# Optimization experiments

Hardware: AMD Instinct MI355X
Metric: run time of the kernel (lower is better)

Reference implementation:

```python
import jax, jax.numpy as jnp
import numpy as np

N = 50000      # nodes
E = 800000     # edges (avg degree 16)
B = 8          # graphs in batch
H = 128        # hidden (message_passer out_channels)
FF = 64        # fourier_feat_dim -> fourier features have dim 2*FF
REPEATS = 4    # repeats_training
OUT = 4        # output_dim
IN_X = 5
IN_MASK = 3

def _fourier(x, M):
    # https://arxiv.org/pdf/2106.02795.pdf : [cos(xM), sin(xM)] / sqrt(2F)
    p = x @ M
    return jnp.concatenate([jnp.cos(p), jnp.sin(p)], axis=-1) / jnp.sqrt(2.0 * M.shape[1])

def _seg_mean(v, idx, n):
    s = jax.ops.segment_sum(v, idx, num_segments=n)
    c = jax.ops.segment_sum(jnp.ones((v.shape[0],), v.dtype), idx, num_segments=n)
    return s / jnp.maximum(c, 1.0)[:, None]

def setup_inputs() -> dict:
    key = jax.random.key(0)
    ks = jax.random.split(key, 16)
    x = jax.random.normal(ks[0], (N, IN_X), jnp.float32)
    x_mask = jax.random.bernoulli(ks[1], 0.1, (N, IN_MASK)).astype(jnp.float32)
    edge_index = jax.random.randint(ks[2], (2, E), 0, N)
    edge_attr = jax.random.normal(ks[3], (E, 3), jnp.float32)
    pos = jax.random.uniform(ks[4], (N, 2), jnp.float32)
    batch = jnp.sort(jax.random.randint(ks[5], (N,), 0, B))
    sampling_points = jax.random.uniform(ks[6], (2,), jnp.float32)
    fourier_mat = jax.random.normal(ks[7], (2, FF), jnp.float32)  # learnable, init N(0,1)
    W_enc = jax.random.normal(ks[8], (IN_X + IN_MASK, H), jnp.float32) * 0.1
    b_enc = jnp.zeros((H,), jnp.float32)
    W_msg = jax.random.normal(ks[9], (2 * H + 3, H), jnp.float32) * 0.05
    b_msg = jnp.zeros((H,), jnp.float32)
    W_upd = jax.random.normal(ks[10], (4 * H, H), jnp.float32) * 0.05
    b_upd = jnp.zeros((H,), jnp.float32)
    W_dec = jax.random.normal(ks[11], (H, OUT), jnp.float32) * 0.1
    b_dec = jnp.zeros((OUT,), jnp.float32)
    return dict(x=x, x_mask=x_mask, edge_index=edge_index, edge_attr=edge_attr,
                pos=pos, batch=batch, sampling_points=sampling_points,
                fourier_mat=fourier_mat, W_enc=W_enc, b_enc=b_enc,
                W_msg=W_msg, b_msg=b_msg, W_upd=W_upd, b_upd=b_upd,
                W_dec=W_dec, b_dec=b_dec)

def reference(x, x_mask, edge_index, edge_attr, pos, batch, sampling_points,
              fourier_mat, W_enc, b_enc, W_msg, b_msg, W_upd, b_upd, W_dec, b_dec):
    bc = x_mask[:, -1]                                   # 0/1 BC flag
    x_full = jnp.concatenate([x, x_mask], axis=1)        # x = concat([x, x_mask])
    keys_ff = _fourier(pos, fourier_mat)                 # input fourier features [N, 2F]
    h = jax.nn.relu(x_full @ W_enc + b_enc)              # encoder -> [N, H]

    # x_BC: scatter-mean over BC nodes per graph (computed once)
    bc_sum = jax.ops.segment_sum(h * bc[:, None], batch, num_segments=B)
    bc_cnt = jax.ops.segment_sum(bc, batch, num_segments=B)
    x_BC = bc_sum / jnp.maximum(bc_cnt, 1.0)[:, None]    # [B, H]

    x_graph = _seg_mean(h, batch, B)                     # global_mean_pool [B, H]
    src, dst = edge_index[0], edge_index[1]
    deg = jnp.maximum(jax.ops.segment_sum(jnp.ones((E,), h.dtype), dst, num_segments=N), 1.0)

    for _ in range(REPEATS):  # repeated message passing
        m = jax.nn.relu(jnp.concatenate([h[src], h[dst], edge_attr], axis=1) @ W_msg + b_msg)
        agg = jax.ops.segment_sum(m, dst, num_segments=N) / deg[:, None]  # scatter-mean
        upd_in = jnp.concatenate([h, agg, x_graph[batch], x_BC[batch]], axis=1)
        h = h + jax.nn.relu(upd_in @ W_upd + b_upd)
        x_graph = _seg_mean(h, batch, B)                 # re-pool each repeat

    decoded = h @ W_dec + b_dec                          # [N, OUT]

    # kernelized fourier-feature interpolation at the sampling point
    q = _fourier(sampling_points, fourier_mat)           # [2F]
    nq = q / jnp.linalg.norm(q)
    nk = keys_ff / jnp.linalg.norm(keys_ff, axis=1, keepdims=True)
    vals_sum = h.sum(axis=0)                             # [H]
    kwv = nk.T @ h                                       # [2F, H]
    ks_sum = nk.sum(axis=0)                              # [2F]
    enc = (vals_sum + nq @ kwv) / (N + nq @ ks_sum)      # [H]
    U_sampled = enc @ W_dec + b_dec                      # [OUT]
    # pack (U_sampled, decoded) into one array: row 0 = sampled point, rows 1: = nodes
    return jnp.concatenate([U_sampled[None, :], decoded], axis=0)
```

## Files before the change

kernel.cpp:

```cpp
#include <hip/hip_runtime.h>
#include <math.h>

#define Nn 50000
#define Ee 800000
#define Bb 8
#define ROUNDS 4
#define KWVB 512
#define SCB 196
#define AP 40
#define HP 132
#define KS 40

typedef __attribute__((ext_vector_type(8))) short bf16x8;
typedef __attribute__((ext_vector_type(4))) float f32x4;

__device__ inline short f2bf(float f) {
  union { float f; unsigned u; } v; v.f = f;
  unsigned r = v.u + 0x7fff + ((v.u >> 16) & 1);
  return (short)(r >> 16);
}
__device__ inline float bf2f(short s) {
  union { float f; unsigned u; } v; v.u = ((unsigned)(unsigned short)s) << 16;
  return v.f;
}

__global__ __launch_bounds__(256) void encode_seg(
    const float* __restrict__ x, const float* __restrict__ xm,
    const int* __restrict__ batch, const float* __restrict__ W,
    const float* __restrict__ b, float* __restrict__ h,
    float* __restrict__ gsum, float* __restrict__ gcnt,
    float* __restrict__ bcsum, float* __restrict__ bccnt) {
  __shared__ float xs5[128 * 5];
  __shared__ float xm3[128 * 3];
  __shared__ float ls[Bb * 128];
  __shared__ float lb[Bb * 128];
  __shared__ float lc[Bb], lbc[Bb];
  const int t = threadIdx.x;
  const int nBase = blockIdx.x * 128;
  const int j = t & 127, half = t >> 7;
  const int base5 = nBase * 5, base3 = nBase * 3;
  for (int q = t; q < 640; q += 256) xs5[q] = (base5 + q < Nn * 5) ? x[base5 + q] : 0.f;
  for (int q = t; q < 384; q += 256) xm3[q] = (base3 + q < Nn * 3) ? xm[base3 + q] : 0.f;
  for (int q = t; q < Bb * 128; q += 256) { ls[q] = 0.f; lb[q] = 0.f; }
  if (t < Bb) { lc[t] = 0.f; lbc[t] = 0.f; }
  float Wcol[8];
#pragma unroll
  for (int k = 0; k < 8; k++) Wcol[k] = W[k * 128 + j];
  const float bj = b[j];
  __syncthreads();
  int curb = -1;
  float runh = 0.f, runb = 0.f, runc = 0.f, runbc = 0.f;
  for (int kk = 0; kk < 64; kk++) {
    int i = nBase + kk * 2 + half;
    if (i >= Nn) break;
    int li = i - nBase;
    float acc = bj;
#pragma unroll
    for (int k = 0; k < 5; k++) acc = fmaf(xs5[li * 5 + k], Wcol[k], acc);
#pragma unroll
    for (int k = 0; k < 3; k++) acc = fmaf(xm3[li * 3 + k], Wcol[5 + k], acc);
    float v = fmaxf(acc, 0.f);
    h[(size_t)i * 128 + j] = v;
    float bc = xm3[li * 3 + 2];
    int g = batch[i];
    if (g != curb) {
      if (curb >= 0) {
        atomicAdd(&ls[curb * 128 + j], runh);
        atomicAdd(&lb[curb * 128 + j], runb);
        if (j == 0) { atomicAdd(&lc[curb], runc); atomicAdd(&lbc[curb], runbc); }
      }
      curb = g; runh = runb = runc = runbc = 0.f;
    }
    runh += v; runb += v * bc;
    if (j == 0) { runc += 1.f; runbc += bc; }
  }
  if (curb >= 0) {
    atomicAdd(&ls[curb * 128 + j], runh);
    atomicAdd(&lb[curb * 128 + j], runb);
    if (j == 0) { atomicAdd(&lc[curb], runc); atomicAdd(&lbc[curb], runbc); }
  }
  __syncthreads();
  for (int q = t; q < Bb * 128; q += 256) {
    float a = ls[q], c = lb[q];
    if (a != 0.f) atomicAdd(&gsum[q], a);
    if (c != 0.f) atomicAdd(&bcsum[q], c);
  }
  if (t < Bb) { atomicAdd(&gcnt[t], lc[t]); atomicAdd(&bccnt[t], lbc[t]); }
}

__global__ __launch_bounds__(256) void split_w_kernel(
    const float* __restrict__ Wm, const float* __restrict__ Wu,
    short* __restrict__ Wmt_h, short* __restrict__ Wmt_l,
    short* __restrict__ Wut_h, short* __restrict__ Wut_l) {
  int idx = blockIdx.x * 256 + threadIdx.x;
  if (idx < 32768) {
    int k = idx & 127, n = (idx >> 7) & 127, y = idx >> 14;
    float w = Wm[(size_t)(y * 128 + k) * 128 + n];
    short hi = f2bf(w);
    Wmt_h[idx] = hi;
    Wmt_l[idx] = f2bf(w - bf2f(hi));
  } else if (idx < 65536) {
    int j = idx - 32768;
    int k = j & 255, n = j >> 8;
    float w = Wu[(size_t)k * 128 + n];
    short hi = f2bf(w);
    Wut_h[j] = hi;
    Wut_l[j] = f2bf(w - bf2f(hi));
  }
}

__global__ void cnt_kernel(const int* __restrict__ ei, int* __restrict__ cnt) {
  int e = blockIdx.x * 256 + threadIdx.x;
  if (e < Ee) atomicAdd(&cnt[ei[Ee + e]], 1);
}
__global__ __launch_bounds__(256) void bsum_kernel(const int* __restrict__ cnt,
                                                   int* __restrict__ bsum) {
  __shared__ int wsum[4];
  int t = threadIdx.x;
  int i = blockIdx.x * 256 + t;
  int v = (i < Nn) ? cnt[i] : 0;
#pragma unroll
  for (int off = 32; off > 0; off >>= 1) v += __shfl_down(v, off);
  if ((t & 63) == 0) wsum[t >> 6] = v;
  __syncthreads();
  if (t == 0) bsum[blockIdx.x] = wsum[0] + wsum[1] + wsum[2] + wsum[3];
}
__global__ __launch_bounds__(256) void scan_top_kernel(const int* __restrict__ bsum,
                                                       int* __restrict__ boff) {
  __shared__ int s[256];
  int t = threadIdx.x;
  int v = (t < SCB) ? bsum[t] : 0;
  s[t] = v;
  __syncthreads();
  for (int off = 1; off < 256; off <<= 1) {
    int x = (t >= off) ? s[t - off] : 0;
    __syncthreads();
    s[t] += x;
    __syncthreads();
  }
  boff[t] = s[t] - v;
}
__global__ __launch_bounds__(256) void apply_kernel(
    const int* __restrict__ cnt, const int* __restrict__ boff,
    int* __restrict__ cursor, int* __restrict__ rowptr,
    float* __restrict__ invdeg) {
  __shared__ int s[256];
  int t = threadIdx.x;
  int i = blockIdx.x * 256 + t;
  int v = (i < Nn) ? cnt[i] : 0;
  s[t] = v;
  __syncthreads();
  for (int off = 1; off < 256; off <<= 1) {
    int x = (t >= off) ? s[t - off] : 0;
    __syncthreads();
    s[t] += x;
    __syncthreads();
  }
  int ex = boff[blockIdx.x] + s[t] - v;
  if (i < Nn) {
    cursor[i] = ex;
    rowptr[i] = ex;
    invdeg[i] = 1.0f / fmaxf((float)v, 1.0f);
    if (i == Nn - 1) rowptr[Nn] = ex + v;
  }
}
__global__ void scatter_kernel(const int* __restrict__ ei, const float* __restrict__ ea,
                               int* __restrict__ cursor, int2* __restrict__ rec) {
  int e = blockIdx.x * 256 + threadIdx.x;
  if (e < Ee) {
    int d = ei[Ee + e];
    int p = atomicAdd(&cursor[d], 1);
    unsigned r0 = (unsigned)ei[e] |
                  ((unsigned)(unsigned short)f2bf(ea[3 * (size_t)e + 0]) << 16);
    unsigned r1 = (unsigned)(unsigned short)f2bf(ea[3 * (size_t)e + 1]) |
                  ((unsigned)(unsigned short)f2bf(ea[3 * (size_t)e + 2]) << 16);
    rec[p] = make_int2((int)r0, (int)r1);
  }
}

__global__ __launch_bounds__(128) void gb_static_kernel(
    const float* __restrict__ bcsum, const float* __restrict__ bccnt,
    const float* __restrict__ Wu, const float* __restrict__ bu,
    float* __restrict__ gbst) {
  __shared__ float xb[128];
  int g = blockIdx.x, t = threadIdx.x;
  xb[t] = bcsum[g * 128 + t] / fmaxf(bccnt[g], 1.f);
  __syncthreads();
  float acc = bu[t];
#pragma unroll 4
  for (int k = 0; k < 128; k++) acc = fmaf(xb[k], Wu[(size_t)(384 + k) * 128 + t], acc);
  gbst[g * 128 + t] = acc;
}

__global__ __launch_bounds__(128) void gb_dyn_kernel(
    const float* __restrict__ gsum, const float* __restrict__ gcnt,
    const float* __restrict__ gbst, const float* __restrict__ Wu,
    float* __restrict__ gb) {
  __shared__ float xg[128];
  int g = blockIdx.x, t = threadIdx.x;
  xg[t] = gsum[g * 128 + t] / fmaxf(gcnt[g], 1.f);
  __syncthreads();
  float acc = gbst[g * 128 + t];
#pragma unroll 4
  for (int k = 0; k < 128; k++) acc = fmaf(xg[k], Wu[(size_t)(256 + k) * 128 + t], acc);
  gb[g * 128 + t] = acc;
}

__global__ __launch_bounds__(256) void proj_mfma(
    const float* __restrict__ h, const short* __restrict__ Wth,
    const short* __restrict__ Wtl, unsigned char* __restrict__ hs8,
    unsigned short* __restrict__ hdbf) {
  __shared__ short Ah_s[128 * AP], Al_s[128 * AP];
  __shared__ short Bh_s[128 * AP], Bl_s[128 * AP];
  const int t = threadIdx.x;
  const int nBase = blockIdx.x * 128;
  const int yoff = blockIdx.y * 16384;
  const int wave = t >> 6, lane = t & 63;
  const int ml = lane & 15, quad = lane >> 4;
  const int ko = quad * 8;

  f32x4 acc[2][8];
#pragma unroll
  for (int nt = 0; nt < 2; nt++)
#pragma unroll
    for (int mt = 0; mt < 8; mt++)
#pragma unroll
      for (int q = 0; q < 4; q++) acc[nt][mt][q] = 0.f;

  const int srow = t >> 1;
  const int kc = (t & 1) * 16;
  const int nd0 = nBase + srow;
  const int nn = nd0 < Nn ? nd0 : Nn - 1;

  for (int c = 0; c < 4; c++) {
    const float* p = &h[(size_t)nn * 128 + c * 32 + kc];
    float4 u0 = *(const float4*)(p + 0);
    float4 u1 = *(const float4*)(p + 4);
    float4 u2 = *(const float4*)(p + 8);
    float4 u3 = *(const float4*)(p + 12);
    const int k0 = c * 32;
    const bf16x8 gb0 = *(const bf16x8*)&Wth[(size_t)yoff + srow * 128 + k0 + kc];
    const bf16x8 gb1 = *(const bf16x8*)&Wth[(size_t)yoff + srow * 128 + k0 + kc + 8];
    const bf16x8 gl0 = *(const bf16x8*)&Wtl[(size_t)yoff + srow * 128 + k0 + kc];
    const bf16x8 gl1 = *(const bf16x8*)&Wtl[(size_t)yoff + srow * 128 + k0 + kc + 8];
    float xs[16] = {u0.x,u0.y,u0.z,u0.w, u1.x,u1.y,u1.z,u1.w,
                    u2.x,u2.y,u2.z,u2.w, u3.x,u3.y,u3.z,u3.w};
    bf16x8 vh0, vh1, vl0, vl1;
#pragma unroll
    for (int j = 0; j < 8; j++) {
      short hi = f2bf(xs[j]);
      vh0[j] = hi; vl0[j] = f2bf(xs[j] - bf2f(hi));
    }
#pragma unroll
    for (int j = 0; j < 8; j++) {
      short hi = f2bf(xs[8 + j]);
      vh1[j] = hi; vl1[j] = f2bf(xs[8 + j] - bf2f(hi));
    }
    __syncthreads();
    *(bf16x8*)&Ah_s[srow * AP + kc] = vh0;
    *(bf16x8*)&Ah_s[srow * AP + kc + 8] = vh1;
    *(bf16x8*)&Al_s[srow * AP + kc] = vl0;
    *(bf16x8*)&Al_s[srow * AP + kc + 8] = vl1;
    *(bf16x8*)&Bh_s[srow * AP + kc] = gb0;
    *(bf16x8*)&Bh_s[srow * AP + kc + 8] = gb1;
    *(bf16x8*)&Bl_s[srow * AP + kc] = gl0;
    *(bf16x8*)&Bl_s[srow * AP + kc + 8] = gl1;
    __syncthreads();
#pragma unroll
    for (int mt = 0; mt < 8; mt++) {
      const int ar = (mt * 16 + ml) * AP + ko;
      bf16x8 ah = *(const bf16x8*)&Ah_s[ar];
      bf16x8 al = *(const bf16x8*)&Al_s[ar];
#pragma unroll
      for (int nt = 0; nt < 2; nt++) {
        const int br = (wave * 32 + nt * 16 + ml) * AP + ko;
        bf16x8 bh = *(const bf16x8*)&Bh_s[br];
        bf16x8 bl = *(const bf16x8*)&Bl_s[br];
        acc[nt][mt] = __builtin_amdgcn_mfma_f32_16x16x32_bf16(ah, bh, acc[nt][mt], 0, 0, 0);
        acc[nt][mt] = __builtin_amdgcn_mfma_f32_16x16x32_bf16(ah, bl, acc[nt][mt], 0, 0, 0);
        acc[nt][mt] = __builtin_amdgcn_mfma_f32_16x16x32_bf16(al, bh, acc[nt][mt], 0, 0, 0);
      }
    }
  }
  if (blockIdx.y == 0) {
#pragma unroll
    for (int nt = 0; nt < 2; nt++) {
      const int ch = wave * 32 + nt * 16 + ml;
#pragma unroll
      for (int mt = 0; mt < 8; mt++) {
#pragma unroll
        for (int q = 0; q < 4; q++) {
          int nd = nBase + mt * 16 + quad * 4 + q;
          if (nd < Nn) {
            int pk = __builtin_amdgcn_cvt_pk_fp8_f32(acc[nt][mt][q], acc[nt][mt][q], 0, false);
            hs8[(size_t)nd * 128 + ch] = (unsigned char)(pk & 0xff);
          }
        }
      }
    }
  } else {
#pragma unroll
    for (int nt = 0; nt < 2; nt++) {
      const int ch = wave * 32 + nt * 16 + ml;
#pragma unroll
      for (int mt = 0; mt < 8; mt++) {
#pragma unroll
        for (int q = 0; q < 4; q++) {
          int nd = nBase + mt * 16 + quad * 4 + q;
          if (nd < Nn) hdbf[(size_t)nd * 128 + ch] = (unsigned short)f2bf(acc[nt][mt][q]);
        }
      }
    }
  }
}

__global__ __launch_bounds__(256) void agg_kernel(
    const unsigned char* __restrict__ hs8, const unsigned short* __restrict__ hdbf,
    unsigned short* __restrict__ aggbf, const int2* __restrict__ rec,
    const int* __restrict__ rowptr, const float* __restrict__ invdeg,
    const float* __restrict__ Wm, const float* __restrict__ bm) {
  int t = threadIdx.x;
  int hw = t >> 5, lane = t & 31;
  int v = blockIdx.x * 8 + hw;
  if (v >= Nn) return;
  int c0 = lane * 4;
  const float4 We0 = *(const float4*)&Wm[(size_t)256 * 128 + c0];
  const float4 We1 = *(const float4*)&Wm[(size_t)257 * 128 + c0];
  const float4 We2 = *(const float4*)&Wm[(size_t)258 * 128 + c0];
  const float4 b4  = *(const float4*)&bm[c0];
  const ushort4 hd4 = *(const ushort4*)&hdbf[(size_t)v * 128 + c0];
  const float bx = b4.x + bf2f((short)hd4.x), by = b4.y + bf2f((short)hd4.y),
              bz = b4.z + bf2f((short)hd4.z), bw = b4.w + bf2f((short)hd4.w);
  float ax = 0.f, ay = 0.f, az = 0.f, aw = 0.f;
  float ax2 = 0.f, ay2 = 0.f, az2 = 0.f, aw2 = 0.f;
  const int r0 = rowptr[v], r1 = rowptr[v + 1];
  int e = r0;
  for (; e + 2 <= r1; e += 2) {
    int2 q0 = rec[e], q1 = rec[e + 1];
    int s0 = q0.x & 0xffff, s1 = q1.x & 0xffff;
    unsigned hr0 = *(const unsigned*)&hs8[(size_t)s0 * 128 + c0];
    unsigned hr1 = *(const unsigned*)&hs8[(size_t)s1 * 128 + c0];
    float e00 = bf2f((short)(q0.x >> 16));
    float e01 = bf2f((short)(q0.y & 0xffff));
    float e02 = bf2f((short)(q0.y >> 16));
    float e10 = bf2f((short)(q1.x >> 16));
    float e11 = bf2f((short)(q1.y & 0xffff));
    float e12 = bf2f((short)(q1.y >> 16));
    float h0x = __builtin_amdgcn_cvt_f32_fp8(hr0, 0);
    float h0y = __builtin_amdgcn_cvt_f32_fp8(hr0, 1);
    float h0z = __builtin_amdgcn_cvt_f32_fp8(hr0, 2);
    float h0w = __builtin_amdgcn_cvt_f32_fp8(hr0, 3);
    float h1x = __builtin_amdgcn_cvt_f32_fp8(hr1, 0);
    float h1y = __builtin_amdgcn_cvt_f32_fp8(hr1, 1);
    float h1z = __builtin_amdgcn_cvt_f32_fp8(hr1, 2);
    float h1w = __builtin_amdgcn_cvt_f32_fp8(hr1, 3);
    ax += fmaxf(fmaf(e00, We0.x, fmaf(e01, We1.x, fmaf(e02, We2.x, h0x + bx))), 0.f);
    ay += fmaxf(fmaf(e00, We0.y, fmaf(e01, We1.y, fmaf(e02, We2.y, h0y + by))), 0.f);
    az += fmaxf(fmaf(e00, We0.z, fmaf(e01, We1.z, fmaf(e02, We2.z, h0z + bz))), 0.f);
    aw += fmaxf(fmaf(e00, We0.w, fmaf(e01, We1.w, fmaf(e02, We2.w, h0w + bw))), 0.f);
    ax2 += fmaxf(fmaf(e10, We0.x, fmaf(e11, We1.x, fmaf(e12, We2.x, h1x + bx))), 0.f);
    ay2 += fmaxf(fmaf(e10, We0.y, fmaf(e11, We1.y, fmaf(e12, We2.y, h1y + by))), 0.f);
    az2 += fmaxf(fmaf(e10, We0.z, fmaf(e11, We1.z, fmaf(e12, We2.z, h1z + bz))), 0.f);
    aw2 += fmaxf(fmaf(e10, We0.w, fmaf(e11, We1.w, fmaf(e12, We2.w, h1w + bw))), 0.f);
  }
  if (e < r1) {
    int2 q0 = rec[e];
    int s0 = q0.x & 0xffff;
    unsigned hr0 = *(const unsigned*)&hs8[(size_t)s0 * 128 + c0];
    float e00 = bf2f((short)(q0.x >> 16));
    float e01 = bf2f((short)(q0.y & 0xffff));
    float e02 = bf2f((short)(q0.y >> 16));
    float h0x = __builtin_amdgcn_cvt_f32_fp8(hr0, 0);
    float h0y = __builtin_amdgcn_cvt_f32_fp8(hr0, 1);
    float h0z = __builtin_amdgcn_cvt_f32_fp8(hr0, 2);
    float h0w = __builtin_amdgcn_cvt_f32_fp8(hr0, 3);
    ax += fmaxf(fmaf(e00, We0.x, fmaf(e01, We1.x, fmaf(e02, We2.x, h0x + bx))), 0.f);
    ay += fmaxf(fmaf(e00, We0.y, fmaf(e01, We1.y, fmaf(e02, We2.y, h0y + by))), 0.f);
    az += fmaxf(fmaf(e00, We0.z, fmaf(e01, We1.z, fmaf(e02, We2.z, h0z + bz))), 0.f);
    aw += fmaxf(fmaf(e00, We0.w, fmaf(e01, We1.w, fmaf(e02, We2.w, h0w + bw))), 0.f);
  }
  const float idg = invdeg[v];
  ushort4 o;
  o.x = (unsigned short)f2bf((ax + ax2) * idg);
  o.y = (unsigned short)f2bf((ay + ay2) * idg);
  o.z = (unsigned short)f2bf((az + az2) * idg);
  o.w = (unsigned short)f2bf((aw + aw2) * idg);
  *(ushort4*)&aggbf[(size_t)v * 128 + c0] = o;
}

__global__ __launch_bounds__(256) void updg_mfma(
    float* __restrict__ h, const unsigned short* __restrict__ aggbf,
    const int* __restrict__ batch,
    const short* __restrict__ Wth, const short* __restrict__ Wtl,
    const float* __restrict__ gb, float* __restrict__ gsum_out) {
  __shared__ short Ah_s[128 * AP], Al_s[128 * AP];
  __shared__ short Bh_s[128 * AP], Bl_s[128 * AP];
  __shared__ float gbs[Bb * 128];
  __shared__ float ls[Bb * 128];
  const int t = threadIdx.x;
  const int nBase = blockIdx.x * 128;
  *(float4*)&gbs[t * 4] = *(const float4*)&gb[t * 4];
#pragma unroll
  for (int q = 0; q < 4; q++) ls[t + q * 256] = 0.f;

  const int wave = t >> 6, lane = t & 63;
  const int ml = lane & 15, quad = lane >> 4;
  const int ko = quad * 8;

  f32x4 acc[2][8];
#pragma unroll
  for (int nt = 0; nt < 2; nt++)
#pragma unroll
    for (int mt = 0; mt < 8; mt++)
#pragma unroll
      for (int q = 0; q < 4; q++) acc[nt][mt][q] = 0.f;

  const int srow = t >> 1;
  const int kc = (t & 1) * 16;
  const int nd0 = nBase + srow;
  const int nn = nd0 < Nn ? nd0 : Nn - 1;

  for (int c = 0; c < 8; c++) {
    const int k0 = c * 32;
    bf16x8 vh0, vh1, vl0, vl1;
    if (c < 4) {
      const float* p = &h[(size_t)nn * 128 + c * 32 + kc];
      float4 u0 = *(const float4*)(p + 0);
      float4 u1 = *(const float4*)(p + 4);
      float4 u2 = *(const float4*)(p + 8);
      float4 u3 = *(const float4*)(p + 12);
      float xs[16] = {u0.x,u0.y,u0.z,u0.w, u1.x,u1.y,u1.z,u1.w,
                      u2.x,u2.y,u2.z,u2.w, u3.x,u3.y,u3.z,u3.w};
#pragma unroll
      for (int j = 0; j < 8; j++) {
        short hi = f2bf(xs[j]);
        vh0[j] = hi; vl0[j] = f2bf(xs[j] - bf2f(hi));
      }
#pragma unroll
      for (int j = 0; j < 8; j++) {
        short hi = f2bf(xs[8 + j]);
        vh1[j] = hi; vl1[j] = f2bf(xs[8 + j] - bf2f(hi));
      }
    } else {
      const unsigned short* pa = &aggbf[(size_t)nn * 128 + (c - 4) * 32 + kc];
      vh0 = *(const bf16x8*)(pa);
      vh1 = *(const bf16x8*)(pa + 8);
    }
    const bf16x8 gb0 = *(const bf16x8*)&Wth[(size_t)srow * 256 + k0 + kc];
    const bf16x8 gb1 = *(const bf16x8*)&Wth[(size_t)srow * 256 + k0 + kc + 8];
    const bf16x8 gl0 = *(const bf16x8*)&Wtl[(size_t)srow * 256 + k0 + kc];
    const bf16x8 gl1 = *(const bf16x8*)&Wtl[(size_t)srow * 256 + k0 + kc + 8];
    __syncthreads();
    *(bf16x8*)&Ah_s[srow * AP + kc] = vh0;
    *(bf16x8*)&Ah_s[srow * AP + kc + 8] = vh1;
    if (c < 4) {
      *(bf16x8*)&Al_s[srow * AP + kc] = vl0;
      *(bf16x8*)&Al_s[srow * AP + kc + 8] = vl1;
    }
    *(bf16x8*)&Bh_s[srow * AP + kc] = gb0;
    *(bf16x8*)&Bh_s[srow * AP + kc + 8] = gb1;
    *(bf16x8*)&Bl_s[srow * AP + kc] = gl0;
    *(bf16x8*)&Bl_s[srow * AP + kc + 8] = gl1;
    __syncthreads();
    if (c < 4) {
#pragma unroll
      for (int mt = 0; mt < 8; mt++) {
        const int ar = (mt * 16 + ml) * AP + ko;
        bf16x8 ah = *(const bf16x8*)&Ah_s[ar];
        bf16x8 al = *(const bf16x8*)&Al_s[ar];
#pragma unroll
        for (int nt = 0; nt < 2; nt++) {
          const int br = (wave * 32 + nt * 16 + ml) * AP + ko;
          bf16x8 bh = *(const bf16x8*)&Bh_s[br];
          bf16x8 bl = *(const bf16x8*)&Bl_s[br];
          acc[nt][mt] = __builtin_amdgcn_mfma_f32_16x16x32_bf16(ah, bh, acc[nt][mt], 0, 0, 0);
          acc[nt][mt] = __builtin_amdgcn_mfma_f32_16x16x32_bf16(ah, bl, acc[nt][mt], 0, 0, 0);
          acc[nt][mt] = __builtin_amdgcn_mfma_f32_16x16x32_bf16(al, bh, acc[nt][mt], 0, 0, 0);
        }
      }
    } else {
#pragma unroll
      for (int mt = 0; mt < 8; mt++) {
        const int ar = (mt * 16 + ml) * AP + ko;
        bf16x8 ah = *(const bf16x8*)&Ah_s[ar];
#pragma unroll
        for (int nt = 0; nt < 2; nt++) {
          const int br = (wave * 32 + nt * 16 + ml) * AP + ko;
          bf16x8 bh = *(const bf16x8*)&Bh_s[br];
          bf16x8 bl = *(const bf16x8*)&Bl_s[br];
          acc[nt][mt] = __builtin_amdgcn_mfma_f32_16x16x32_bf16(ah, bh, acc[nt][mt], 0, 0, 0);
          acc[nt][mt] = __builtin_amdgcn_mfma_f32_16x16x32_bf16(ah, bl, acc[nt][mt], 0, 0, 0);
        }
      }
    }
  }
#pragma unroll
  for (int nt = 0; nt < 2; nt++) {
    const int ch = wave * 32 + nt * 16 + ml;
#pragma unroll
    for (int mt = 0; mt < 8; mt++) {
      int rbase = nBase + mt * 16 + quad * 4;
      float runv = 0.f;
      int curb = -1;
#pragma unroll
      for (int q = 0; q < 4; q++) {
        int nd = rbase + q;
        if (nd < Nn) {
          int bi = batch[nd];
          float u = fmaxf(acc[nt][mt][q] + gbs[bi * 128 + ch], 0.f);
          float hn = h[(size_t)nd * 128 + ch] + u;
          h[(size_t)nd * 128 + ch] = hn;
          if (bi != curb) {
            if (curb >= 0) atomicAdd(&ls[curb * 128 + ch], runv);
            curb = bi;
            runv = 0.f;
          }
          runv += hn;
        }
      }
      if (curb >= 0) atomicAdd(&ls[curb * 128 + ch], runv);
    }
  }
  __syncthreads();
#pragma unroll
  for (int q = 0; q < 4; q++) {
    int idx = t + q * 256;
    float v = ls[idx];
    if (v != 0.f) atomicAdd(&gsum_out[idx], v);
  }
}

__global__ __launch_bounds__(256) void kwv_kernel(
    const float* __restrict__ h, const float* __restrict__ pos,
    const float* __restrict__ Fm, const float* __restrict__ Wd,
    const float* __restrict__ bd, float* __restrict__ partial,
    float* __restrict__ ksum, float* __restrict__ out) {
  __shared__ float h_s[32 * HP];
  __shared__ short nkT[128 * KS];
  __shared__ short hT[128 * KS];
  __shared__ float wd[512];
  __shared__ float ksum_s[128];
  const int t = threadIdx.x;
  const int hr = t >> 3;
  const int hc = (t & 7) * 16;
  const int fg = (t & 7) * 8;
  const int wave = t >> 6, lane = t & 63;
  const int ml = lane & 15, quad = lane >> 4;
  const int ko = quad * 8;
  if (t < 128) { *(float4*)&wd[t * 4] = *(const float4*)&Wd[t * 4]; ksum_s[t] = 0.f; }
  const float bdv = bd[t & 3];
  f32x4 acc[2][8];
#pragma unroll
  for (int nt = 0; nt < 2; nt++)
#pragma unroll
    for (int mt = 0; mt < 8; mt++)
#pragma unroll
      for (int q = 0; q < 4; q++) acc[nt][mt][q] = 0.f;
  float klc[8], kls[8];
#pragma unroll
  for (int f = 0; f < 8; f++) { klc[f] = 0.f; kls[f] = 0.f; }

  const int nTiles = (Nn + 31) / 32;
  for (int tile = blockIdx.x; tile < nTiles; tile += gridDim.x) {
    const int gh = tile * 32 + hr;
    float4 hv0 = {0.f, 0.f, 0.f, 0.f}, hv1 = hv0, hv2 = hv0, hv3 = hv0;
    float cbuf[8], sbuf[8];
    if (gh < Nn) {
      const float* hp = &h[(size_t)gh * 128 + hc];
      hv0 = *(const float4*)(hp + 0);
      hv1 = *(const float4*)(hp + 4);
      hv2 = *(const float4*)(hp + 8);
      hv3 = *(const float4*)(hp + 12);
      const float px = pos[gh * 2 + 0], py = pos[gh * 2 + 1];
#pragma unroll
      for (int f = 0; f < 8; f++) {
        float p = px * Fm[fg + f] + py * Fm[64 + fg + f];
        cbuf[f] = cosf(p) * 0.125f;
        sbuf[f] = sinf(p) * 0.125f;
      }
    } else {
#pragma unroll
      for (int f = 0; f < 8; f++) { cbuf[f] = 0.f; sbuf[f] = 0.f; }
    }
    float xs[16] = {hv0.x,hv0.y,hv0.z,hv0.w, hv1.x,hv1.y,hv1.z,hv1.w,
                    hv2.x,hv2.y,hv2.z,hv2.w, hv3.x,hv3.y,hv3.z,hv3.w};
    __syncthreads();
    *(float4*)&h_s[hr * HP + hc + 0]  = hv0;
    *(float4*)&h_s[hr * HP + hc + 4]  = hv1;
    *(float4*)&h_s[hr * HP + hc + 8]  = hv2;
    *(float4*)&h_s[hr * HP + hc + 12] = hv3;
#pragma unroll
    for (int i = 0; i < 16; i++) hT[(hc + i) * KS + hr] = f2bf(xs[i]);
#pragma unroll
    for (int f = 0; f < 8; f++) {
      nkT[(fg + f) * KS + hr] = f2bf(cbuf[f]);
      nkT[(64 + fg + f) * KS + hr] = f2bf(sbuf[f]);
      klc[f] += cbuf[f];
      kls[f] += sbuf[f];
    }
    __syncthreads();
#pragma unroll
    for (int mt = 0; mt < 8; mt++) {
      bf16x8 ah = *(const bf16x8*)&nkT[(mt * 16 + ml) * KS + ko];
#pragma unroll
      for (int nt = 0; nt < 2; nt++) {
        bf16x8 bh = *(const bf16x8*)&hT[(wave * 32 + nt * 16 + ml) * KS + ko];
        acc[nt][mt] = __builtin_amdgcn_mfma_f32_16x16x32_bf16(ah, bh, acc[nt][mt], 0, 0, 0);
      }
    }
    if (t < 128) {
      int n = t >> 2, o = t & 3;
      int gn = tile * 32 + n;
      if (gn < Nn) {
        float s = bdv;
#pragma unroll 4
        for (int kk = 0; kk < 128; kk++) {
          int k = (kk + n) & 127;
          s = fmaf(h_s[n * HP + k], wd[k * 4 + o], s);
        }
        out[4 + (size_t)gn * 4 + o] = s;
      }
    }
  }
  float* pb = &partial[(size_t)blockIdx.x * 16384];
#pragma unroll
  for (int nt = 0; nt < 2; nt++) {
    const int col = wave * 32 + nt * 16 + ml;
#pragma unroll
    for (int mt = 0; mt < 8; mt++) {
#pragma unroll
      for (int q = 0; q < 4; q++) {
        int row = mt * 16 + quad * 4 + q;
        pb[row * 128 + col] = acc[nt][mt][q];
      }
    }
  }
#pragma unroll
  for (int f = 0; f < 8; f++) {
    atomicAdd(&ksum_s[fg + f], klc[f]);
    atomicAdd(&ksum_s[64 + fg + f], kls[f]);
  }
  __syncthreads();
  if (t < 128) atomicAdd(&ksum[t], ksum_s[t]);
}

__global__ __launch_bounds__(256) void kwv_reduce(const float* __restrict__ partial,
                                                  float* __restrict__ kwv) {
  int idx = blockIdx.x * 256 + threadIdx.x;
  float s = 0.f;
  for (int b = 0; b < KWVB; b++) s += partial[(size_t)b * 16384 + idx];
  kwv[idx] = s;
}

__global__ __launch_bounds__(128) void final_kernel(
    const float* __restrict__ sp, const float* __restrict__ Fm,
    const float* __restrict__ kwv, const float* __restrict__ vs,
    const float* __restrict__ ksum, const float* __restrict__ Wd,
    const float* __restrict__ bd, float* __restrict__ out) {
  __shared__ float nq_s[128];
  __shared__ float red[2];
  __shared__ float redU[8];
  int t = threadIdx.x;
  int jj = t & 63;
  float p = sp[0] * Fm[jj] + sp[1] * Fm[64 + jj];
  nq_s[t] = ((t < 64) ? cosf(p) : sinf(p)) * 0.125f;
  __syncthreads();
  float num = 0.f;
#pragma unroll
  for (int g = 0; g < Bb; g++) num += vs[g * 128 + t];
  for (int k = 0; k < 128; k++) num = fmaf(nq_s[k], kwv[k * 128 + t], num);
  float dp = nq_s[t] * ksum[t];
#pragma unroll
  for (int off = 32; off > 0; off >>= 1) dp += __shfl_down(dp, off);
  if ((t & 63) == 0) red[t >> 6] = dp;
  __syncthreads();
  float den = (float)Nn + red[0] + red[1];
  float e = num / den;
  float u[4];
#pragma unroll
  for (int o = 0; o < 4; o++) u[o] = e * Wd[t * 4 + o];
#pragma unroll
  for (int off = 32; off > 0; off >>= 1) {
#pragma unroll
    for (int o = 0; o < 4; o++) u[o] += __shfl_down(u[o], off);
  }
  if ((t & 63) == 0) {
#pragma unroll
    for (int o = 0; o < 4; o++) redU[(t >> 6) * 4 + o] = u[o];
  }
  __syncthreads();
  if (t < 4) out[t] = redU[t] + redU[4 + t] + bd[t];
}

extern "C" void kernel_launch(void* const* d_in, const int* in_sizes, int n_in,
                              void* d_out, int out_size, void* d_ws, size_t ws_size,
                              hipStream_t stream) {
  const float* x    = (const float*)d_in[0];
  const float* xm   = (const float*)d_in[1];
  const int*   ei   = (const int*)d_in[2];
  const float* ea   = (const float*)d_in[3];
  const float* pos  = (const float*)d_in[4];
  const int*   batch= (const int*)d_in[5];
  const float* sp   = (const float*)d_in[6];
  const float* Fm   = (const float*)d_in[7];
  const float* Wenc = (const float*)d_in[8];
  const float* benc = (const float*)d_in[9];
  const float* Wmsg = (const float*)d_in[10];
  const float* bmsg = (const float*)d_in[11];
  const float* Wupd = (const float*)d_in[12];
  const float* bupd = (const float*)d_in[13];
  const float* Wdec = (const float*)d_in[14];
  const float* bdec = (const float*)d_in[15];
  float* out = (float*)d_out;

  float* ws     = (float*)d_ws;
  float* h      = ws;
  float* agg    = h + (size_t)Nn * 128;
  float* aux    = agg + (size_t)Nn * 128;
  float* invdeg = aux + (size_t)Nn * 128;
  float* gsum   = invdeg + Nn;
  float* gcnt   = gsum + 1024;
  float* bcsum  = gcnt + 8;
  float* bccnt  = bcsum + 1024;
  float* gsumR  = bccnt + 8;
  float* vsum   = gsumR + 4096;
  float* ksum   = vsum + 128;
  float* gbst   = ksum + 128;
  float* gbuf   = gbst + 1024;
  float* kwv    = gbuf + 4096;
  int2*  rec    = (int2*)(kwv + 16384);
  int*   cnt    = (int*)(rec + Ee);
  int*   cursor = cnt + Nn;
  int*   rowptr = cursor + Nn;
  int*   bsum   = rowptr + Nn + 1;
  int*   boff   = bsum + 256;
  short* wmt_h  = (short*)(boff + 256);
  short* wmt_l  = wmt_h + 32768;
  short* wut_h  = wmt_l + 32768;
  short* wut_l  = wut_h + 32768;

  unsigned short* aggbf = (unsigned short*)agg;
  unsigned char*  hs8   = (unsigned char*)aux;
  unsigned short* hdbf  = (unsigned short*)(hs8 + (size_t)Nn * 128);

  hipMemsetAsync(gsum, 0, 6416 * sizeof(float), stream);
  hipMemsetAsync(cnt, 0, Nn * sizeof(int), stream);

  split_w_kernel<<<256, 256, 0, stream>>>(Wmsg, Wupd, wmt_h, wmt_l, wut_h, wut_l);

  cnt_kernel<<<(Ee + 255) / 256, 256, 0, stream>>>(ei, cnt);
  bsum_kernel<<<SCB, 256, 0, stream>>>(cnt, bsum);
  scan_top_kernel<<<1, 256, 0, stream>>>(bsum, boff);
  apply_kernel<<<SCB, 256, 0, stream>>>(cnt, boff, cursor, rowptr, invdeg);
  scatter_kernel<<<(Ee + 255) / 256, 256, 0, stream>>>(ei, ea, cursor, rec);

  const int nb128 = (Nn + 127) / 128;
  encode_seg<<<nb128, 256, 0, stream>>>(x, xm, batch, Wenc, benc, h,
                                        gsum, gcnt, bcsum, bccnt);
  gb_static_kernel<<<Bb, 128, 0, stream>>>(bcsum, bccnt, Wupd, bupd, gbst);
  gb_dyn_kernel<<<Bb, 128, 0, stream>>>(gsum, gcnt, gbst, Wupd, gbuf);

  for (int r = 0; r < ROUNDS; r++) {
    proj_mfma<<<dim3(nb128, 2), 256, 0, stream>>>(h, wmt_h, wmt_l, hs8, hdbf);
    agg_kernel<<<(Nn + 7) / 8, 256, 0, stream>>>(hs8, hdbf, aggbf, rec, rowptr,
                                                 invdeg, Wmsg, bmsg);
    updg_mfma<<<nb128, 256, 0, stream>>>(h, aggbf, batch, wut_h, wut_l,
                                         gbuf + r * 1024, gsumR + r * 1024);
    if (r < ROUNDS - 1)
      gb_dyn_kernel<<<Bb, 128, 0, stream>>>(gsumR + r * 1024, gcnt, gbst, Wupd,
                                            gbuf + (r + 1) * 1024);
  }

  kwv_kernel<<<KWVB, 256, 0, stream>>>(h, pos, Fm, Wdec, bdec, agg, ksum, out);
  kwv_reduce<<<64, 256, 0, stream>>>(agg, kwv);
  final_kernel<<<1, 128, 0, stream>>>(sp, Fm, kwv, gsumR + 3 * 1024, ksum,
                                      Wdec, bdec, out);
}
```

Before: 723.4 us.

## Build CSR via two-level bucket partition with shared-memory histograms

Replaces the global-atomic per-destination count and scatter with a two-pass radix-style partition. Edges are first grouped into 256-node buckets using block-local shared histograms, then each bucket is sorted to its destination rows using shared-memory cursors. This is meant to remove the heavy contention and random global atomics of the original CSR build. In exchange it adds several kernel launches and an extra intermediate record buffer plus byte array of traffic.

```diff
diff --git a/kernel.cpp b/kernel.cpp
--- a/kernel.cpp
+++ b/kernel.cpp
@@ -10,6 +10,9 @@
 #define AP 40
 #define HP 132
 #define KS 40
+#define NBK 196
+#define P1B 391
+#define CHUNK 2047
 
 typedef __attribute__((ext_vector_type(8))) short bf16x8;
 typedef __attribute__((ext_vector_type(4))) float f32x4;
@@ -109,27 +112,25 @@
   }
 }
 
-__global__ void cnt_kernel(const int* __restrict__ ei, int* __restrict__ cnt) {
-  int e = blockIdx.x * 256 + threadIdx.x;
-  if (e < Ee) atomicAdd(&cnt[ei[Ee + e]], 1);
-}
-__global__ __launch_bounds__(256) void bsum_kernel(const int* __restrict__ cnt,
-                                                   int* __restrict__ bsum) {
-  __shared__ int wsum[4];
-  int t = threadIdx.x;
-  int i = blockIdx.x * 256 + t;
-  int v = (i < Nn) ? cnt[i] : 0;
-#pragma unroll
-  for (int off = 32; off > 0; off >>= 1) v += __shfl_down(v, off);
-  if ((t & 63) == 0) wsum[t >> 6] = v;
-  __syncthreads();
-  if (t == 0) bsum[blockIdx.x] = wsum[0] + wsum[1] + wsum[2] + wsum[3];
-}
-__global__ __launch_bounds__(256) void scan_top_kernel(const int* __restrict__ bsum,
-                                                       int* __restrict__ boff) {
+__global__ __launch_bounds__(256) void bkt_cnt(const int* __restrict__ ei,
+                                               int* __restrict__ bktcnt) {
+  __shared__ int hist[NBK];
+  int t = threadIdx.x;
+  for (int q = t; q < NBK; q += 256) hist[q] = 0;
+  __syncthreads();
+  int base = blockIdx.x * CHUNK;
+  int end = base + CHUNK < Ee ? base + CHUNK : Ee;
+  for (int e = base + t; e < end; e += 256) atomicAdd(&hist[ei[Ee + e] >> 8], 1);
+  __syncthreads();
+  for (int q = t; q < NBK; q += 256)
+    if (hist[q]) atomicAdd(&bktcnt[q], hist[q]);
+}
+__global__ __launch_bounds__(256) void bkt_scan(const int* __restrict__ bktcnt,
+                                                int* __restrict__ bktbase,
+                                                int* __restrict__ bktcur) {
   __shared__ int s[256];
   int t = threadIdx.x;
-  int v = (t < SCB) ? bsum[t] : 0;
+  int v = (t < NBK) ? bktcnt[t] : 0;
   s[t] = v;
   __syncthreads();
   for (int off = 1; off < 256; off <<= 1) {
@@ -138,43 +139,118 @@
     s[t] += x;
     __syncthreads();
   }
-  boff[t] = s[t] - v;
-}
-__global__ __launch_bounds__(256) void apply_kernel(
-    const int* __restrict__ cnt, const int* __restrict__ boff,
-    int* __restrict__ cursor, int* __restrict__ rowptr,
-    float* __restrict__ invdeg) {
-  __shared__ int s[256];
-  int t = threadIdx.x;
-  int i = blockIdx.x * 256 + t;
-  int v = (i < Nn) ? cnt[i] : 0;
-  s[t] = v;
-  __syncthreads();
-  for (int off = 1; off < 256; off <<= 1) {
-    int x = (t >= off) ? s[t - off] : 0;
-    __syncthreads();
-    s[t] += x;
-    __syncthreads();
-  }
-  int ex = boff[blockIdx.x] + s[t] - v;
-  if (i < Nn) {
-    cursor[i] = ex;
-    rowptr[i] = ex;
-    invdeg[i] = 1.0f / fmaxf((float)v, 1.0f);
-    if (i == Nn - 1) rowptr[Nn] = ex + v;
-  }
-}
-__global__ void scatter_kernel(const int* __restrict__ ei, const float* __restrict__ ea,
-                               int* __restrict__ cursor, int2* __restrict__ rec) {
-  int e = blockIdx.x * 256 + threadIdx.x;
-  if (e < Ee) {
+  int ex = s[t] - v;
+  if (t < NBK) { bktbase[t] = ex; bktcur[t] = ex; }
+  if (t == NBK - 1) bktbase[NBK] = ex + v;
+}
+__global__ __launch_bounds__(256) void bkt_part(
+    const int* __restrict__ ei, const float* __restrict__ ea,
+    int* __restrict__ bktcur, int2* __restrict__ recA,
+    unsigned char* __restrict__ dlo) {
+  __shared__ int hist[NBK], lbase[NBK], lcur[NBK];
+  int t = threadIdx.x;
+  for (int q = t; q < NBK; q += 256) hist[q] = 0;
+  __syncthreads();
+  int base = blockIdx.x * CHUNK;
+  int end = base + CHUNK < Ee ? base + CHUNK : Ee;
+  for (int e = base + t; e < end; e += 256) atomicAdd(&hist[ei[Ee + e] >> 8], 1);
+  __syncthreads();
+  for (int q = t; q < NBK; q += 256) {
+    int c = hist[q];
+    lbase[q] = c ? atomicAdd(&bktcur[q], c) : 0;
+    lcur[q] = 0;
+  }
+  __syncthreads();
+  for (int e = base + t; e < end; e += 256) {
     int d = ei[Ee + e];
-    int p = atomicAdd(&cursor[d], 1);
+    int bk = d >> 8;
+    int p = lbase[bk] + atomicAdd(&lcur[bk], 1);
     unsigned r0 = (unsigned)ei[e] |
                   ((unsigned)(unsigned short)f2bf(ea[3 * (size_t)e + 0]) << 16);
     unsigned r1 = (unsigned)(unsigned short)f2bf(ea[3 * (size_t)e + 1]) |
                   ((unsigned)(unsigned short)f2bf(ea[3 * (size_t)e + 2]) << 16);
-    rec[p] = make_int2((int)r0, (int)r1);
+    recA[p] = make_int2((int)r0, (int)r1);
+    dlo[p] = (unsigned char)(d & 255);
+  }
+}
+__global__ __launch_bounds__(256) void dst_cnt(const int* __restrict__ bktbase,
+                                               const unsigned char* __restrict__ dlo,
+                                               int* __restrict__ cnt) {
+  __shared__ int hh[256];
+  int t = threadIdx.x;
+  hh[t] = 0;
+  __syncthreads();
+  int b = blockIdx.x;
+  int lo = bktbase[b], hi = bktbase[b + 1];
+  for (int i = lo + t; i < hi; i += 256) atomicAdd(&hh[dlo[i]], 1);
+  __syncthreads();
+  int d = b * 256 + t;
+  if (d < Nn) cnt[d] = hh[t];
+}
+__global__ __launch_bounds__(256) void bsum_kernel(const int* __restrict__ cnt,
+                                                   int* __restrict__ bsum) {
+  __shared__ int wsum[4];
+  int t = threadIdx.x;
+  int i = blockIdx.x * 256 + t;
+  int v = (i < Nn) ? cnt[i] : 0;
+#pragma unroll
+  for (int off = 32; off > 0; off >>= 1) v += __shfl_down(v, off);
+  if ((t & 63) == 0) wsum[t >> 6] = v;
+  __syncthreads();
+  if (t == 0) bsum[blockIdx.x] = wsum[0] + wsum[1] + wsum[2] + wsum[3];
+}
+__global__ __launch_bounds__(256) void scan_top_kernel(const int* __restrict__ bsum,
+                                                       int* __restrict__ boff) {
+  __shared__ int s[256];
+  int t = threadIdx.x;
+  int v = (t < SCB) ? bsum[t] : 0;
+  s[t] = v;
+  __syncthreads();
+  for (int off = 1; off < 256; off <<= 1) {
+    int x = (t >= off) ? s[t - off] : 0;
+    __syncthreads();
+    s[t] += x;
+    __syncthreads();
+  }
+  boff[t] = s[t] - v;
+}
+__global__ __launch_bounds__(256) void apply_kernel(
+    const int* __restrict__ cnt, const int* __restrict__ boff,
+    int* __restrict__ rowptr, float* __restrict__ invdeg) {
+  __shared__ int s[256];
+  int t = threadIdx.x;
+  int i = blockIdx.x * 256 + t;
+  int v = (i < Nn) ? cnt[i] : 0;
+  s[t] = v;
+  __syncthreads();
+  for (int off = 1; off < 256; off <<= 1) {
+    int x = (t >= off) ? s[t - off] : 0;
+    __syncthreads();
+    s[t] += x;
+    __syncthreads();
+  }
+  int ex = boff[blockIdx.x] + s[t] - v;
+  if (i < Nn) {
+    rowptr[i] = ex;
+    invdeg[i] = 1.0f / fmaxf((float)v, 1.0f);
+    if (i == Nn - 1) rowptr[Nn] = ex + v;
+  }
+}
+__global__ __launch_bounds__(256) void bkt_fin(
+    const int* __restrict__ bktbase, const int2* __restrict__ recA,
+    const unsigned char* __restrict__ dlo, const int* __restrict__ rowptr,
+    int2* __restrict__ rec) {
+  __shared__ int cur[256];
+  int t = threadIdx.x;
+  int b = blockIdx.x;
+  int d = b * 256 + t;
+  cur[t] = (d < Nn) ? rowptr[d] : 0;
+  __syncthreads();
+  int lo = bktbase[b], hi = bktbase[b + 1];
+  for (int i = lo + t; i < hi; i += 256) {
+    int dl = dlo[i];
+    int p = atomicAdd(&cur[dl], 1);
+    rec[p] = recA[i];
   }
 }
 
@@ -730,29 +806,36 @@
   float* kwv    = gbuf + 4096;
   int2*  rec    = (int2*)(kwv + 16384);
   int*   cnt    = (int*)(rec + Ee);
-  int*   cursor = cnt + Nn;
-  int*   rowptr = cursor + Nn;
+  int*   rowptr = cnt + Nn;
   int*   bsum   = rowptr + Nn + 1;
   int*   boff   = bsum + 256;
-  short* wmt_h  = (short*)(boff + 256);
+  int*   bktcnt = boff + 256;
+  int*   bktbase= bktcnt + 196;
+  int*   bktcur = bktbase + 197;
+  short* wmt_h  = (short*)(bktcur + 196);
   short* wmt_l  = wmt_h + 32768;
   short* wut_h  = wmt_l + 32768;
   short* wut_l  = wut_h + 32768;
+  int2*  recA   = (int2*)(wut_l + 32768);
+  unsigned char* dlo = (unsigned char*)(recA + Ee);
 
   unsigned short* aggbf = (unsigned short*)agg;
   unsigned char*  hs8   = (unsigned char*)aux;
   unsigned short* hdbf  = (unsigned short*)(hs8 + (size_t)Nn * 128);
 
   hipMemsetAsync(gsum, 0, 6416 * sizeof(float), stream);
-  hipMemsetAsync(cnt, 0, Nn * sizeof(int), stream);
+  hipMemsetAsync(bktcnt, 0, 196 * sizeof(int), stream);
 
   split_w_kernel<<<256, 256, 0, stream>>>(Wmsg, Wupd, wmt_h, wmt_l, wut_h, wut_l);
 
-  cnt_kernel<<<(Ee + 255) / 256, 256, 0, stream>>>(ei, cnt);
+  bkt_cnt<<<P1B, 256, 0, stream>>>(ei, bktcnt);
+  bkt_scan<<<1, 256, 0, stream>>>(bktcnt, bktbase, bktcur);
+  bkt_part<<<P1B, 256, 0, stream>>>(ei, ea, bktcur, recA, dlo);
+  dst_cnt<<<NBK, 256, 0, stream>>>(bktbase, dlo, cnt);
   bsum_kernel<<<SCB, 256, 0, stream>>>(cnt, bsum);
   scan_top_kernel<<<1, 256, 0, stream>>>(bsum, boff);
-  apply_kernel<<<SCB, 256, 0, stream>>>(cnt, boff, cursor, rowptr, invdeg);
-  scatter_kernel<<<(Ee + 255) / 256, 256, 0, stream>>>(ei, ea, cursor, rec);
+  apply_kernel<<<SCB, 256, 0, stream>>>(cnt, boff, rowptr, invdeg);
+  bkt_fin<<<NBK, 256, 0, stream>>>(bktbase, recA, dlo, rowptr, rec);
 
   const int nb128 = (Nn + 127) / 128;
   encode_seg<<<nb128, 256, 0, stream>>>(x, xm, batch, Wenc, benc, h,
```

Result: faster. 708.8 us (-2.0%).
